# Kernel optimization log

Measured on AMD Instinct MI355X. Metric: run time of the kernel, lower is better.

The kernel has to match this reference:

```python
import jax, jax.numpy as jnp
import numpy as np

EMBED_DIM = 1024
N_HEADS = 16
HEAD_DIM = EMBED_DIM // N_HEADS
B, T = 4, 2048


def setup_inputs() -> dict:
    key = jax.random.key(0)
    ks = jax.random.split(key, 5)
    s = 1.0 / np.sqrt(EMBED_DIM)
    return {
        "x": jax.random.normal(ks[0], (B, T, EMBED_DIM), dtype=jnp.float32),
        "w_qkv": jax.random.normal(ks[1], (EMBED_DIM, 3 * EMBED_DIM), dtype=jnp.float32) * s,
        "b_qkv": jnp.zeros((3 * EMBED_DIM,), dtype=jnp.float32),
        "w_out": jax.random.normal(ks[2], (EMBED_DIM, EMBED_DIM), dtype=jnp.float32) * s,
        "b_out": jnp.zeros((EMBED_DIM,), dtype=jnp.float32),
    }


def reference(x, w_qkv, b_qkv, w_out, b_out):
    Bb, Tt, C = x.shape
    qkv = x @ w_qkv + b_qkv                      # (B, T, 3C)
    q, k, v = jnp.split(qkv, 3, axis=-1)
    # (B, H, T, Dh)
    def to_heads(t):
        return t.reshape(Bb, Tt, N_HEADS, HEAD_DIM).transpose(0, 2, 1, 3)
    q, k, v = to_heads(q), to_heads(k), to_heads(v)
    scale = 1.0 / np.sqrt(HEAD_DIM)
    scores = jnp.einsum("bhqd,bhkd->bhqk", q, k) * scale  # (B, H, T, T)
    causal = jnp.tril(jnp.ones((Tt, Tt), dtype=bool))
    scores = jnp.where(causal[None, None], scores, -jnp.inf)
    attn = jax.nn.softmax(scores, axis=-1)
    out = jnp.einsum("bhqk,bhkd->bhqd", attn, v)  # (B, H, T, Dh)
    out = out.transpose(0, 2, 1, 3).reshape(Bb, Tt, C)
    return out @ w_out + b_out
```

## Files before the change

kernel.cpp:

```cpp
#include <hip/hip_runtime.h>

typedef __bf16 bf16;
typedef __bf16 bf16x4 __attribute__((ext_vector_type(4)));
typedef __bf16 bf16x8 __attribute__((ext_vector_type(8)));
typedef float f32x4 __attribute__((ext_vector_type(4)));

#define TSEQ 2048
#define NHEAD 16

#define QSCALE 0.18033688011112042f

#if __has_builtin(__builtin_amdgcn_exp2f)
#define EXP2F(x) __builtin_amdgcn_exp2f(x)
#else
#define EXP2F(x) exp2f(x)
#endif

__device__ __forceinline__ void gload_lds16(const bf16* g, bf16* s) {
  __builtin_amdgcn_global_load_lds(
      (const __attribute__((address_space(1))) void*)g,
      (__attribute__((address_space(3))) void*)s, 16, 0, 0);
}

__global__ __launch_bounds__(256) void prep_kernel(
    const float* __restrict__ x, bf16* __restrict__ xbf,
    const float* __restrict__ w_qkv, bf16* __restrict__ wqkvt,
    const float* __restrict__ w_out, bf16* __restrict__ woutt) {
  __shared__ float tile[32][33];
  const int bid = blockIdx.x;
  const int tid = threadIdx.x;
  if (bid < 4096) {
    size_t i = ((size_t)bid * 256 + tid) * 8;
    float4 v0 = ((const float4*)(x + i))[0];
    float4 v1 = ((const float4*)(x + i))[1];
    bf16x8 o;
    o[0] = (bf16)v0.x; o[1] = (bf16)v0.y; o[2] = (bf16)v0.z; o[3] = (bf16)v0.w;
    o[4] = (bf16)v1.x; o[5] = (bf16)v1.y; o[6] = (bf16)v1.z; o[7] = (bf16)v1.w;
    *(bf16x8*)(xbf + i) = o;
    return;
  }
  const float* in; bf16* out; int K, N, n0, k0;
  if (bid < 7168) {
    int q = bid - 4096;
    in = w_qkv; out = wqkvt; K = 1024; N = 3072;
    n0 = (q % 96) * 32; k0 = (q / 96) * 32;
  } else {
    int q = bid - 7168;
    in = w_out; out = woutt; K = 1024; N = 1024;
    n0 = (q & 31) * 32; k0 = (q >> 5) * 32;
  }
  int tx = tid & 31, ty = tid >> 5;
#pragma unroll
  for (int i = ty; i < 32; i += 8)
    tile[i][tx] = in[(size_t)(k0 + i) * N + n0 + tx];
  __syncthreads();
#pragma unroll
  for (int i = ty; i < 32; i += 8)
    out[(size_t)(n0 + i) * K + k0 + tx] = (bf16)tile[tx][i];
}

template <typename OutT, int BN, bool SWZ>
__global__ __launch_bounds__(256, 4) void gemm_bf16_kernel(
    const bf16* __restrict__ A, const bf16* __restrict__ Bt,
    const float* __restrict__ bias, OutT* __restrict__ C,
    int M, int N, int K, int ldc, float scale0, int scale_cols,
    bf16* __restrict__ vp) {
  constexpr int BG = BN / 32;
  constexpr int JN = BN / 32;
  alignas(16) __shared__ bf16 As[128 * 64];
  alignas(16) __shared__ bf16 Bs[BN * 64];

  int bx, by;
  if (SWZ) {
    const int nwg = gridDim.x * gridDim.y;
    const int orig = blockIdx.y * gridDim.x + blockIdx.x;
    const int xcd = orig & 7, qch = nwg >> 3;
    const int wgid = xcd * qch + (orig >> 3);
    bx = wgid % gridDim.x; by = wgid / gridDim.x;
  } else {
    bx = blockIdx.x; by = blockIdx.y;
  }

  const int row0 = by * 128, col0 = bx * BN;
  const int tid = threadIdx.x;
  const int wave = tid >> 6, lane = tid & 63;
  const int quad = lane >> 4, lm = lane & 15;
  const int wm = (wave >> 1) * 64, wn = (wave & 1) * (BN / 2);

  f32x4 acc[4][JN];
  const f32x4 z4 = {0.0f, 0.0f, 0.0f, 0.0f};
#pragma unroll
  for (int i = 0; i < 4; i++)
#pragma unroll
    for (int j = 0; j < JN; j++) acc[i][j] = z4;

  const int sr0 = tid >> 3;
  const int js = (tid & 7) ^ ((tid >> 4) & 7);
  const bf16* apg = A + (size_t)(row0 + sr0) * K + js * 8;
  const bf16* bpg = Bt + (size_t)(col0 + sr0) * K + js * 8;
  const size_t row32 = (size_t)32 * K;

  const int sw = (lm >> 1) & 7;

  for (int k0 = 0; k0 < K; k0 += 64) {
    __syncthreads();
#pragma unroll
    for (int p = 0; p < 4; p++)
      gload_lds16(apg + p * row32, &As[(p * 256 + tid) * 8]);
#pragma unroll
    for (int p = 0; p < BG; p++)
      gload_lds16(bpg + p * row32, &Bs[(p * 256 + tid) * 8]);
    apg += 64; bpg += 64;
    __syncthreads();

#pragma unroll
    for (int ks = 0; ks < 2; ks++) {
      const int kc = ((ks * 4 + quad) ^ sw) * 8;
      bf16x8 af[4], bfr[JN];
#pragma unroll
      for (int i = 0; i < 4; i++)
        af[i] = *(const bf16x8*)&As[(wm + i * 16 + lm) * 64 + kc];
#pragma unroll
      for (int j = 0; j < JN; j++)
        bfr[j] = *(const bf16x8*)&Bs[(wn + j * 16 + lm) * 64 + kc];
#pragma unroll
      for (int i = 0; i < 4; i++)
#pragma unroll
        for (int j = 0; j < JN; j++)
          acc[i][j] = __builtin_amdgcn_mfma_f32_16x16x32_bf16(af[i], bfr[j], acc[i][j], 0, 0, 0);
    }
  }

#pragma unroll
  for (int j = 0; j < JN; j++) {
    int gc = col0 + wn + j * 16 + lm;
    float bb = bias[gc];
    float sc2 = (gc < scale_cols) ? scale0 : 1.0f;
    if (vp != nullptr && gc >= 2048) {
      int gr0 = row0 + wm + quad * 4;
      int b = gr0 >> 11;
      size_t vrow = (size_t)(b * 1024 + gc - 2048) * TSEQ;
#pragma unroll
      for (int i = 0; i < 4; i++) {
        int t = (gr0 + i * 16) & (TSEQ - 1);
        bf16x4 vk;
#pragma unroll
        for (int rr = 0; rr < 4; rr++) vk[rr] = (bf16)(acc[i][j][rr] + bb);
        *(bf16x4*)(vp + vrow + t) = vk;
      }
    } else {
#pragma unroll
      for (int i = 0; i < 4; i++) {
        int gr = row0 + wm + i * 16 + quad * 4;
#pragma unroll
        for (int rr = 0; rr < 4; rr++) {
          float v = (acc[i][j][rr] + bb) * sc2;
          C[(size_t)(gr + rr) * ldc + gc] = (OutT)v;
        }
      }
    }
  }
}

__global__ __launch_bounds__(256, 4) void flash_attn_kernel(
    const bf16* __restrict__ qk, const bf16* __restrict__ vp,
    bf16* __restrict__ att) {
  alignas(16) __shared__ bf16 Ks[64 * 64];
  alignas(16) __shared__ bf16 Vts[64 * 64];
  alignas(16) __shared__ bf16 Ps[4][32 * 64];

  const int hb = blockIdx.x;
  const int h = hb & 15, b = hb >> 4;
  const int y = blockIdx.y;
  const int g = y >> 2, r = y & 3;
  const int qt = (g == 0) ? (15 - r) : (g == 1) ? r : (g == 2) ? (11 - r) : (4 + r);
  const int q0 = qt * 128;
  const int tid = threadIdx.x;
  const int wave = tid >> 6, lane = tid & 63;
  const int quad = lane >> 4, lm = lane & 15;
  const size_t rowbase = (size_t)b * TSEQ;
  const f32x4 z4 = {0.0f, 0.0f, 0.0f, 0.0f};

  bf16x8 bq[2][2];
#pragma unroll
  for (int nf = 0; nf < 2; nf++)
#pragma unroll
    for (int ks = 0; ks < 2; ks++)
      bq[nf][ks] = *(const bf16x8*)(qk +
          (rowbase + q0 + wave * 32 + nf * 16 + lm) * 2048 + h * 64 + ks * 32 + quad * 8);

  const int strow = tid >> 3;
  const int js = (tid & 7) ^ ((tid >> 4) & 7);
  const bf16* kstg = qk + (rowbase + strow) * 2048 + 1024 + h * 64 + js * 8;
  const bf16* vstg = vp + ((size_t)hb * 64 + strow) * TSEQ + js * 8;
  const size_t krow32 = (size_t)32 * 2048;
  const size_t vrow32 = (size_t)32 * TSEQ;

  const int sw = (lm >> 1) & 7;

  f32x4 oT[4][2];
#pragma unroll
  for (int mf = 0; mf < 4; mf++)
#pragma unroll
    for (int nf = 0; nf < 2; nf++) oT[mf][nf] = z4;
  float lp[2] = {0.0f, 0.0f};

  const int nkt = 2 * qt + 2;
  const int wrow_lo = q0 + wave * 32;
  const int wrow_hi = wrow_lo + 31;

  for (int kt = 0; kt < nkt; kt++) {
    const int k0 = kt * 64;
    __syncthreads();
    gload_lds16(kstg + (size_t)k0 * 2048, &Ks[tid * 8]);
    gload_lds16(kstg + (size_t)k0 * 2048 + krow32, &Ks[(256 + tid) * 8]);
    gload_lds16(vstg + k0, &Vts[tid * 8]);
    gload_lds16(vstg + k0 + vrow32, &Vts[(256 + tid) * 8]);
    __syncthreads();
    if (k0 > wrow_hi) continue;

    f32x4 s[4][2];
#pragma unroll
    for (int mf = 0; mf < 4; mf++)
#pragma unroll
      for (int nf = 0; nf < 2; nf++) s[mf][nf] = z4;
#pragma unroll
    for (int ks = 0; ks < 2; ks++) {
      const int kc = ((ks * 4 + quad) ^ sw) * 8;
      bf16x8 ak[4];
#pragma unroll
      for (int mf = 0; mf < 4; mf++)
        ak[mf] = *(const bf16x8*)&Ks[(mf * 16 + lm) * 64 + kc];
#pragma unroll
      for (int mf = 0; mf < 4; mf++)
#pragma unroll
        for (int nf = 0; nf < 2; nf++)
          s[mf][nf] = __builtin_amdgcn_mfma_f32_16x16x32_bf16(ak[mf], bq[nf][ks], s[mf][nf], 0, 0, 0);
    }

    const bool need_mask = (k0 + 63 > wrow_lo);
#pragma unroll
    for (int nf = 0; nf < 2; nf++) {
      const int qrow = q0 + wave * 32 + nf * 16 + lm;
#pragma unroll
      for (int mf = 0; mf < 4; mf++) {
        bf16x4 pk;
        float psum = 0.0f;
#pragma unroll
        for (int rr = 0; rr < 4; rr++) {
          float pv = EXP2F(s[mf][nf][rr]);
          if (need_mask) {
            int kv = k0 + mf * 16 + quad * 4 + rr;
            pv = (kv > qrow) ? 0.0f : pv;
          }
          psum += pv;
          pk[rr] = (bf16)pv;
        }
        lp[nf] += psum;
        *(bf16x4*)&Ps[wave][(nf * 16 + lm) * 64 +
                            (((mf * 2 + (quad >> 1)) ^ sw) * 8 + (quad & 1) * 4)] = pk;
      }
    }

#pragma unroll
    for (int ks = 0; ks < 2; ks++) {
      const int kc = ((ks * 4 + quad) ^ sw) * 8;
      bf16x8 av[4], bp[2];
#pragma unroll
      for (int mf = 0; mf < 4; mf++)
        av[mf] = *(const bf16x8*)&Vts[(mf * 16 + lm) * 64 + kc];
#pragma unroll
      for (int nf = 0; nf < 2; nf++)
        bp[nf] = *(const bf16x8*)&Ps[wave][(nf * 16 + lm) * 64 + kc];
#pragma unroll
      for (int mf = 0; mf < 4; mf++)
#pragma unroll
        for (int nf = 0; nf < 2; nf++)
          oT[mf][nf] = __builtin_amdgcn_mfma_f32_16x16x32_bf16(av[mf], bp[nf], oT[mf][nf], 0, 0, 0);
    }
  }

  float linv[2];
#pragma unroll
  for (int nf = 0; nf < 2; nf++) {
    float l = lp[nf];
    l += __shfl_xor(l, 16, 64);
    l += __shfl_xor(l, 32, 64);
    linv[nf] = 1.0f / l;
  }

#pragma unroll
  for (int nf = 0; nf < 2; nf++) {
    const size_t grow = rowbase + q0 + wave * 32 + nf * 16 + lm;
#pragma unroll
    for (int mf = 0; mf < 4; mf++) {
      bf16x4 ok;
#pragma unroll
      for (int rr = 0; rr < 4; rr++) ok[rr] = (bf16)(oT[mf][nf][rr] * linv[nf]);
      *(bf16x4*)(att + grow * 1024 + h * 64 + mf * 16 + quad * 4) = ok;
    }
  }
}

extern "C" void kernel_launch(void* const* d_in, const int* in_sizes, int n_in,
                              void* d_out, int out_size, void* d_ws, size_t ws_size,
                              hipStream_t stream) {
  const float* x = (const float*)d_in[0];
  const float* w_qkv = (const float*)d_in[1];
  const float* b_qkv = (const float*)d_in[2];
  const float* w_out = (const float*)d_in[3];
  const float* b_out = (const float*)d_in[4];
  float* out = (float*)d_out;

  char* ws = (char*)d_ws;
  bf16* Xbf   = (bf16*)(ws);
  bf16* ATT   = (bf16*)(ws);
  bf16* Wqkvt = (bf16*)(ws + 16777216);
  bf16* Woutt = (bf16*)(ws + 23068672);
  bf16* QK    = (bf16*)(ws + 25165824);
  bf16* VP    = (bf16*)(ws + 58720256);

  prep_kernel<<<8192, 256, 0, stream>>>(x, Xbf, w_qkv, Wqkvt, w_out, Woutt);
  gemm_bf16_kernel<bf16, 128, false><<<dim3(24, 64), 256, 0, stream>>>(
      Xbf, Wqkvt, b_qkv, QK, 8192, 3072, 1024, 2048, QSCALE, 1024, VP);
  flash_attn_kernel<<<dim3(64, 16, 1), 256, 0, stream>>>(QK, VP, ATT);
  gemm_bf16_kernel<float, 64, true><<<dim3(16, 64), 256, 0, stream>>>(
      ATT, Woutt, b_out, out, 8192, 1024, 1024, 1024, 1.0f, 0, nullptr);
}
```

Baseline: 242.0 us.

## Replace QKV GEMM with 256x256-tile 8-wave kernel using phased LDS prefetch

Adds a dedicated QKV projection GEMM that uses 256x256 output tiles, 512 threads and double-buffered LDS split into halves. Global-to-LDS loads for upcoming k-steps are interleaved across four MFMA phases, with explicit waitcnt, barriers and setprio. The aim is to raise data reuse per tile and hide load latency behind MFMA work. In exchange it uses 128KB of LDS and many accumulator registers per block, which limits occupancy, and the grid is only 384 blocks.

Measured after the change: 261.3 us. 1.08x slower.

```diff
diff --git a/kernel.cpp b/kernel.cpp
--- a/kernel.cpp
+++ b/kernel.cpp
@@ -59,6 +59,123 @@
     out[(size_t)(n0 + i) * K + k0 + tx] = (bf16)tile[tx][i];
 }
 
+__global__ __launch_bounds__(512, 2) void gemm_qkv_8ph(
+    const bf16* __restrict__ A, const bf16* __restrict__ Bt,
+    const float* __restrict__ bias, bf16* __restrict__ C,
+    bf16* __restrict__ vp) {
+  alignas(16) __shared__ bf16 Asl[2][2][128 * 64];
+  alignas(16) __shared__ bf16 Bsl[2][2][128 * 64];
+  const int row0 = blockIdx.y * 256, col0 = blockIdx.x * 256;
+  const int tid = threadIdx.x;
+  const int wave = tid >> 6, lane = tid & 63;
+  const int quad = lane >> 4, lm = lane & 15;
+  const int wr = wave >> 2, wc = wave & 3;
+  const int sw = (lm >> 1) & 7;
+  const int sr = tid >> 3;
+  const int js = (tid & 7) ^ ((tid >> 4) & 7);
+  const bf16* ag = A + (size_t)(row0 + sr) * 1024 + js * 8;
+  const bf16* bg = Bt + (size_t)(col0 + sr) * 1024 + js * 8;
+
+#define STA(d, h, s, kt) gload_lds16(ag + (size_t)((h) * 128 + (s) * 64) * 1024 + (kt) * 64, \
+                                     &Asl[d][h][(s) * 4096 + tid * 8])
+#define STB(d, h, s, kt) gload_lds16(bg + (size_t)((h) * 128 + (s) * 64) * 1024 + (kt) * 64, \
+                                     &Bsl[d][h][(s) * 4096 + tid * 8])
+
+  f32x4 acc[8][4];
+  const f32x4 z4 = {0.0f, 0.0f, 0.0f, 0.0f};
+#pragma unroll
+  for (int i = 0; i < 8; i++)
+#pragma unroll
+    for (int j = 0; j < 4; j++) acc[i][j] = z4;
+
+  STA(0, 0, 0, 0); STA(0, 0, 1, 0);
+  STB(0, 0, 0, 0); STB(0, 0, 1, 0);
+  STA(0, 1, 0, 0); STA(0, 1, 1, 0);
+  STB(0, 1, 0, 0); STB(0, 1, 1, 0);
+  STA(1, 0, 0, 1); STA(1, 0, 1, 1);
+  STB(1, 0, 0, 1); STB(1, 0, 1, 1);
+  asm volatile("s_waitcnt vmcnt(4)" ::: "memory");
+  __builtin_amdgcn_s_barrier();
+  __builtin_amdgcn_sched_barrier(0);
+
+  for (int kt = 0; kt < 16; ++kt) {
+    const int d = kt & 1;
+#pragma unroll
+    for (int q = 0; q < 4; ++q) {
+      const int mh = q >> 1, nh = q & 1;
+      bf16x8 a8[4][2], b8[2][2];
+#pragma unroll
+      for (int mfp = 0; mfp < 4; ++mfp)
+#pragma unroll
+        for (int ks = 0; ks < 2; ++ks)
+          a8[mfp][ks] = *(const bf16x8*)&Asl[d][mh][(wr * 64 + mfp * 16 + lm) * 64 +
+                                                    ((ks * 4 + quad) ^ sw) * 8];
+#pragma unroll
+      for (int nfp = 0; nfp < 2; ++nfp)
+#pragma unroll
+        for (int ks = 0; ks < 2; ++ks)
+          b8[nfp][ks] = *(const bf16x8*)&Bsl[d][nh][(wc * 32 + nfp * 16 + lm) * 64 +
+                                                    ((ks * 4 + quad) ^ sw) * 8];
+      if (q == 0 && kt + 1 < 16) { STA(d ^ 1, 1, 0, kt + 1); STA(d ^ 1, 1, 1, kt + 1); }
+      if (q == 1 && kt + 1 < 16) { STB(d ^ 1, 1, 0, kt + 1); STB(d ^ 1, 1, 1, kt + 1); }
+      if (q == 2 && kt + 2 < 16) { STA(d, 0, 0, kt + 2); STA(d, 0, 1, kt + 2); }
+      if (q == 3 && kt + 2 < 16) { STB(d, 0, 0, kt + 2); STB(d, 0, 1, kt + 2); }
+      __builtin_amdgcn_s_barrier();
+      asm volatile("s_waitcnt lgkmcnt(0)" ::: "memory");
+      __builtin_amdgcn_sched_barrier(0);
+      __builtin_amdgcn_s_setprio(1);
+#pragma unroll
+      for (int mfp = 0; mfp < 4; ++mfp)
+#pragma unroll
+        for (int nfp = 0; nfp < 2; ++nfp)
+#pragma unroll
+          for (int ks = 0; ks < 2; ++ks)
+            acc[mh * 4 + mfp][nh * 2 + nfp] = __builtin_amdgcn_mfma_f32_16x16x32_bf16(
+                a8[mfp][ks], b8[nfp][ks], acc[mh * 4 + mfp][nh * 2 + nfp], 0, 0, 0);
+      __builtin_amdgcn_s_setprio(0);
+      if (q == 3) {
+        if (kt < 14)
+          asm volatile("s_waitcnt vmcnt(4)" ::: "memory");
+        else
+          asm volatile("s_waitcnt vmcnt(0)" ::: "memory");
+      }
+      __builtin_amdgcn_s_barrier();
+      __builtin_amdgcn_sched_barrier(0);
+    }
+  }
+
+#pragma unroll
+  for (int nf = 0; nf < 4; ++nf) {
+    const int gc = col0 + (nf >> 1) * 128 + wc * 32 + (nf & 1) * 16 + lm;
+    const float bb = bias[gc];
+    if (gc >= 2048) {
+      const size_t vbase = (size_t)(gc - 2048) * TSEQ;
+#pragma unroll
+      for (int mf = 0; mf < 8; ++mf) {
+        const int gr0 = row0 + (mf >> 2) * 128 + wr * 64 + (mf & 3) * 16 + quad * 4;
+        const int b = gr0 >> 11;
+        const size_t vrow = (size_t)b * 1024 * TSEQ + vbase;
+        const int t = gr0 & (TSEQ - 1);
+        bf16x4 vk;
+#pragma unroll
+        for (int rr = 0; rr < 4; ++rr) vk[rr] = (bf16)(acc[mf][nf][rr] + bb);
+        *(bf16x4*)(vp + vrow + t) = vk;
+      }
+    } else {
+      const float sc2 = (gc < 1024) ? QSCALE : 1.0f;
+#pragma unroll
+      for (int mf = 0; mf < 8; ++mf) {
+        const int gr0 = row0 + (mf >> 2) * 128 + wr * 64 + (mf & 3) * 16 + quad * 4;
+#pragma unroll
+        for (int rr = 0; rr < 4; ++rr)
+          C[(size_t)(gr0 + rr) * 2048 + gc] = (bf16)((acc[mf][nf][rr] + bb) * sc2);
+      }
+    }
+  }
+#undef STA
+#undef STB
+}
+
 template <typename OutT, int BN, bool SWZ>
 __global__ __launch_bounds__(256, 4) void gemm_bf16_kernel(
     const bf16* __restrict__ A, const bf16* __restrict__ Bt,
@@ -321,8 +438,7 @@
   bf16* VP    = (bf16*)(ws + 58720256);
 
   prep_kernel<<<8192, 256, 0, stream>>>(x, Xbf, w_qkv, Wqkvt, w_out, Woutt);
-  gemm_bf16_kernel<bf16, 128, false><<<dim3(24, 64), 256, 0, stream>>>(
-      Xbf, Wqkvt, b_qkv, QK, 8192, 3072, 1024, 2048, QSCALE, 1024, VP);
+  gemm_qkv_8ph<<<dim3(12, 32), 512, 0, stream>>>(Xbf, Wqkvt, b_qkv, QK, VP);
   flash_attn_kernel<<<dim3(64, 16, 1), 256, 0, stream>>>(QK, VP, ATT);
   gemm_bf16_kernel<float, 64, true><<<dim3(16, 64), 256, 0, stream>>>(
       ATT, Woutt, b_out, out, 8192, 1024, 1024, 1024, 1.0f, 0, nullptr);
```
